# Kernel tuning notes

Measured on AMD Instinct MI355X. Metric: run time of the kernel, lower is better.

## Reference

```python
import jax, jax.numpy as jnp
import numpy as np

B, S, E, H = 4, 1024, 1024, 16
HD = E // H  # head_dim = 64


def setup_inputs() -> dict:
    key = jax.random.key(0)
    ks = jax.random.split(key, 7)
    return {
        "query": jax.random.normal(ks[0], (B, S, E), dtype=jnp.float32),
        "key": jax.random.normal(ks[1], (B, S, E), dtype=jnp.float32),
        "value": jax.random.normal(ks[2], (B, S, E), dtype=jnp.float32),
        # per-head Linear weights stacked: [H, head_dim, emb_dim] (torch Linear is y = x @ W^T)
        "Wq": jax.random.normal(ks[3], (H, HD, E), dtype=jnp.float32) * (E ** -0.5),
        "Wk": jax.random.normal(ks[4], (H, HD, E), dtype=jnp.float32) * (E ** -0.5),
        "Wv": jax.random.normal(ks[5], (H, HD, E), dtype=jnp.float32) * (E ** -0.5),
        "Wo": jax.random.normal(ks[6], (E, E), dtype=jnp.float32) * (E ** -0.5),
    }


def reference(query, key, value, Wq, Wk, Wv, Wo):
    # Project per head (all heads vectorized): [B,S,E] x [H,HD,E] -> [B,H,S,HD]
    Q = jnp.einsum('bse,hde->bhsd', query, Wq)
    K = jnp.einsum('bse,hde->bhsd', key, Wk)
    V = jnp.einsum('bse,hde->bhsd', value, Wv)
    scale = 1.0 / np.sqrt(HD)  # source divides by sqrt(emb_dim / n_head)
    scores = jnp.einsum('bhsd,bhtd->bhst', Q, K) * scale  # [B,H,S,S]
    p = jax.nn.softmax(scores, axis=-1)
    ctx = jnp.einsum('bhst,bhtd->bhsd', p, V)  # [B,H,S,HD]
    # concat heads along feature dim -> [B,S,E]
    concat = ctx.transpose(0, 2, 1, 3).reshape(query.shape[0], query.shape[1], -1)
    return concat @ Wo.T
```

## Files before the change

### kernel.cpp

```cpp
#include <hip/hip_runtime.h>

typedef __bf16 bf16_t;
typedef __bf16 bf16x4 __attribute__((ext_vector_type(4)));
typedef __bf16 bf16x8 __attribute__((ext_vector_type(8)));
typedef float f32x4 __attribute__((ext_vector_type(4)));
typedef short short4v __attribute__((ext_vector_type(4)));

#define E_DIM 1024
#define S_LEN 1024
#define NHEAD 16
#define HD_DIM 64
#define BATCH 4
#define TOKENS 4096

__device__ __forceinline__ void async_copy16(const bf16_t* g, bf16_t* l) {
    __builtin_amdgcn_global_load_lds((const __attribute__((address_space(1))) void*)g,
                                     (__attribute__((address_space(3))) void*)l,
                                     16, 0, 0);
}

__device__ __forceinline__ f32x4 pv_mfma(bf16x4 a, bf16x4 b, f32x4 c) {
#if __has_builtin(__builtin_amdgcn_mfma_f32_16x16x16_bf16)
    return __builtin_amdgcn_mfma_f32_16x16x16_bf16(a, b, c, 0, 0, 0);
#elif __has_builtin(__builtin_amdgcn_mfma_f32_16x16x16bf16_1k)
    short4v as, bs;
    __builtin_memcpy(&as, &a, 8);
    __builtin_memcpy(&bs, &b, 8);
    return __builtin_amdgcn_mfma_f32_16x16x16bf16_1k(as, bs, c, 0, 0, 0);
#else
    f32x4 d;
    asm volatile("v_mfma_f32_16x16x16_bf16 %0, %1, %2, %3\n\ts_nop 7\n\ts_nop 7"
                 : "=v"(d)
                 : "v"(a), "v"(b), "v"(c));
    return d;
#endif
}

__device__ __forceinline__ void stage_tiles(const bf16_t* gA, const bf16_t* gB,
                                            bf16_t* sAbuf, bf16_t* sBbuf,
                                            int wave, int k0) {
    const int K = 1024;
#pragma unroll
    for (int cc = 0; cc < 4; cc++) {
        int c = wave * 4 + cc;
        if (c < 8)
            async_copy16(gA + (size_t)c * 16 * K + k0, sAbuf + c * 16 * 32);
        else
            async_copy16(gB + (size_t)(c - 8) * 16 * K + k0, sBbuf + (c - 8) * 16 * 32);
    }
}

__global__ __launch_bounds__(256) void cast_all(const float* __restrict__ q,
                                                const float* __restrict__ k,
                                                const float* __restrict__ v,
                                                const float* __restrict__ wq,
                                                const float* __restrict__ wk,
                                                const float* __restrict__ wv,
                                                const float* __restrict__ wo,
                                                bf16_t* __restrict__ dst) {
    const size_t NX = (size_t)TOKENS * E_DIM;
    const size_t NW = (size_t)E_DIM * E_DIM;
    size_t i = ((size_t)blockIdx.x * 256 + threadIdx.x) * 8;
    const float* src;
    size_t off;
    if (i < 3 * NX) {
        int a = (int)(i >> 22);
        src = a == 0 ? q : (a == 1 ? k : v);
        off = i & (NX - 1);
    } else {
        size_t j = i - 3 * NX;
        int a = (int)(j >> 20);
        src = a == 0 ? wq : (a == 1 ? wk : (a == 2 ? wv : wo));
        off = j & (NW - 1);
    }
    float4 x = *(const float4*)(src + off);
    float4 y = *(const float4*)(src + off + 4);
    bf16x8 o;
    o[0] = (bf16_t)x.x; o[1] = (bf16_t)x.y; o[2] = (bf16_t)x.z; o[3] = (bf16_t)x.w;
    o[4] = (bf16_t)y.x; o[5] = (bf16_t)y.y; o[6] = (bf16_t)y.z; o[7] = (bf16_t)y.w;
    *(bf16x8*)(dst + i) = o;
}

__global__ __launch_bounds__(256, 3) void proj_gemm(const bf16_t* __restrict__ Xq,
                                                    const bf16_t* __restrict__ Xk,
                                                    const bf16_t* __restrict__ Xv,
                                                    const bf16_t* __restrict__ Wq,
                                                    const bf16_t* __restrict__ Wk,
                                                    const bf16_t* __restrict__ Wv,
                                                    bf16_t* __restrict__ Qp,
                                                    bf16_t* __restrict__ Kp,
                                                    bf16_t* __restrict__ Vp) {
    __shared__ bf16_t sA[3][128 * 32];
    __shared__ bf16_t sB[3][128 * 32];
    const int z = blockIdx.z;
    const bf16_t* A = z == 0 ? Xq : (z == 1 ? Xk : Xv);
    const bf16_t* B = z == 0 ? Wq : (z == 1 ? Wk : Wv);
    bf16_t* C = z == 0 ? Qp : (z == 1 ? Kp : Vp);
    const int N = 1024, K = 1024;
    const int lid = blockIdx.x + 8 * blockIdx.y;
    const int m0 = (((lid & 7) << 2) + ((lid >> 3) & 3)) * 128;
    const int n0 = (lid >> 5) * 128;

    const int tid = threadIdx.x;
    const int wave = tid >> 6, lane = tid & 63;
    const int quad = lane >> 4, l16 = lane & 15;
    const int wm = (wave >> 1) * 64, wn = (wave & 1) * 64;
    const int srow = lane >> 2, scol = (lane & 3) * 8;

    const bf16_t* gA = A + (size_t)(m0 + srow) * K + scol;
    const bf16_t* gB = B + (size_t)(n0 + srow) * K + scol;

    f32x4 acc[4][4];
    const f32x4 vzero = {0.f, 0.f, 0.f, 0.f};
#pragma unroll
    for (int mt = 0; mt < 4; mt++)
#pragma unroll
        for (int nt = 0; nt < 4; nt++) acc[mt][nt] = vzero;

#define PROJ_COMPUTE(cur)                                                             \
    {                                                                                 \
        bf16x8 af[4], bfr[4];                                                         \
        _Pragma("unroll") for (int mt = 0; mt < 4; mt++)                              \
            af[mt] = *(const bf16x8*)&sA[cur][(wm + mt * 16 + l16) * 32 + quad * 8];  \
        _Pragma("unroll") for (int nt = 0; nt < 4; nt++)                              \
            bfr[nt] = *(const bf16x8*)&sB[cur][(wn + nt * 16 + l16) * 32 + quad * 8]; \
        _Pragma("unroll") for (int mt = 0; mt < 4; mt++)                              \
            _Pragma("unroll") for (int nt = 0; nt < 4; nt++)                          \
                acc[mt][nt] = __builtin_amdgcn_mfma_f32_16x16x32_bf16(                \
                    af[mt], bfr[nt], acc[mt][nt], 0, 0, 0);                           \
    }

    stage_tiles(gA, gB, sA[0], sB[0], wave, 0);
    stage_tiles(gA, gB, sA[1], sB[1], wave, 32);
    stage_tiles(gA, gB, sA[2], sB[2], wave, 64);

    int cur = 0;
#pragma unroll 1
    for (int it = 0; it < 29; ++it) {
        asm volatile("s_waitcnt vmcnt(8)" ::: "memory");
        asm volatile("s_barrier" ::: "memory");
        PROJ_COMPUTE(cur);
        asm volatile("s_waitcnt lgkmcnt(0)" ::: "memory");
        asm volatile("s_barrier" ::: "memory");
        stage_tiles(gA, gB, sA[cur], sB[cur], wave, (it + 3) * 32);
        cur = cur == 2 ? 0 : cur + 1;
    }
    asm volatile("s_waitcnt vmcnt(8)" ::: "memory");
    asm volatile("s_barrier" ::: "memory");
    PROJ_COMPUTE(cur);
    cur = cur == 2 ? 0 : cur + 1;
    asm volatile("s_waitcnt vmcnt(4)" ::: "memory");
    asm volatile("s_barrier" ::: "memory");
    PROJ_COMPUTE(cur);
    cur = cur == 2 ? 0 : cur + 1;
    asm volatile("s_waitcnt vmcnt(0)" ::: "memory");
    asm volatile("s_barrier" ::: "memory");
    PROJ_COMPUTE(cur);
#undef PROJ_COMPUTE

#pragma unroll
    for (int mt = 0; mt < 4; mt++)
#pragma unroll
        for (int nt = 0; nt < 4; nt++)
#pragma unroll
            for (int r = 0; r < 4; r++) {
                int row = m0 + wm + mt * 16 + quad * 4 + r;
                int col = n0 + wn + nt * 16 + l16;
                C[(size_t)row * N + col] = (bf16_t)acc[mt][nt][r];
            }
}

__global__ __launch_bounds__(256, 3) void out_gemm(const bf16_t* __restrict__ A,
                                                   const bf16_t* __restrict__ B,
                                                   float* __restrict__ C) {
    __shared__ bf16_t sA[3][128 * 32];
    __shared__ bf16_t sB[3][128 * 32];
    const int N = 1024, K = 1024;
    const int lid = blockIdx.x + 8 * blockIdx.y;
    const int m0 = (((lid & 7) << 2) + ((lid >> 3) & 3)) * 128;
    const int n0 = (lid >> 5) * 128;

    const int tid = threadIdx.x;
    const int wave = tid >> 6, lane = tid & 63;
    const int quad = lane >> 4, l16 = lane & 15;
    const int wm = (wave >> 1) * 64, wn = (wave & 1) * 64;
    const int srow = lane >> 2, scol = (lane & 3) * 8;

    const bf16_t* gA = A + (size_t)(m0 + srow) * K + scol;
    const bf16_t* gB = B + (size_t)(n0 + srow) * K + scol;

    f32x4 acc[4][4];
    const f32x4 vzero = {0.f, 0.f, 0.f, 0.f};
#pragma unroll
    for (int mt = 0; mt < 4; mt++)
#pragma unroll
        for (int nt = 0; nt < 4; nt++) acc[mt][nt] = vzero;

#define OUT_COMPUTE(cur)                                                              \
    {                                                                                 \
        bf16x8 af[4], bfr[4];                                                         \
        _Pragma("unroll") for (int mt = 0; mt < 4; mt++)                              \
            af[mt] = *(const bf16x8*)&sA[cur][(wm + mt * 16 + l16) * 32 + quad * 8];  \
        _Pragma("unroll") for (int nt = 0; nt < 4; nt++)                              \
            bfr[nt] = *(const bf16x8*)&sB[cur][(wn + nt * 16 + l16) * 32 + quad * 8]; \
        _Pragma("unroll") for (int mt = 0; mt < 4; mt++)                              \
            _Pragma("unroll") for (int nt = 0; nt < 4; nt++)                          \
                acc[mt][nt] = __builtin_amdgcn_mfma_f32_16x16x32_bf16(                \
                    af[mt], bfr[nt], acc[mt][nt], 0, 0, 0);                           \
    }

    stage_tiles(gA, gB, sA[0], sB[0], wave, 0);
    stage_tiles(gA, gB, sA[1], sB[1], wave, 32);
    stage_tiles(gA, gB, sA[2], sB[2], wave, 64);

    int cur = 0;
#pragma unroll 1
    for (int it = 0; it < 29; ++it) {
        asm volatile("s_waitcnt vmcnt(8)" ::: "memory");
        asm volatile("s_barrier" ::: "memory");
        OUT_COMPUTE(cur);
        asm volatile("s_waitcnt lgkmcnt(0)" ::: "memory");
        asm volatile("s_barrier" ::: "memory");
        stage_tiles(gA, gB, sA[cur], sB[cur], wave, (it + 3) * 32);
        cur = cur == 2 ? 0 : cur + 1;
    }
    asm volatile("s_waitcnt vmcnt(8)" ::: "memory");
    asm volatile("s_barrier" ::: "memory");
    OUT_COMPUTE(cur);
    cur = cur == 2 ? 0 : cur + 1;
    asm volatile("s_waitcnt vmcnt(4)" ::: "memory");
    asm volatile("s_barrier" ::: "memory");
    OUT_COMPUTE(cur);
    cur = cur == 2 ? 0 : cur + 1;
    asm volatile("s_waitcnt vmcnt(0)" ::: "memory");
    asm volatile("s_barrier" ::: "memory");
    OUT_COMPUTE(cur);
#undef OUT_COMPUTE

#pragma unroll
    for (int mt = 0; mt < 4; mt++)
#pragma unroll
        for (int nt = 0; nt < 4; nt++)
#pragma unroll
            for (int r = 0; r < 4; r++) {
                int row = m0 + wm + mt * 16 + quad * 4 + r;
                int col = n0 + wn + nt * 16 + l16;
                C[(size_t)row * N + col] = acc[mt][nt][r];
            }
}

#define KP 72

__global__ __launch_bounds__(256, 2) void flash_attn(const bf16_t* __restrict__ Q,
                                                     const bf16_t* __restrict__ K,
                                                     const bf16_t* __restrict__ V,
                                                     bf16_t* __restrict__ O) {
    __shared__ bf16_t smem[2 * 64 * KP];
    bf16_t* sK = smem;
    bf16_t* sVt = smem + 64 * KP;

    const int tid = threadIdx.x;
    const int wave = tid >> 6, lane = tid & 63;
    const int quad = lane >> 4, l16 = lane & 15;
    const int qt = blockIdx.y >> 1;
    const int h = blockIdx.x * 2 + (blockIdx.y & 1);
    const int b = blockIdx.z;
    const size_t base = (size_t)b * S_LEN * E_DIM + h * HD_DIM;
    const float c_exp = 0.125f * 1.44269504089f;

    bf16x8 qf[2][2];
#pragma unroll
    for (int mt = 0; mt < 2; mt++) {
        const bf16_t* qp =
            Q + base + (size_t)(qt * 128 + wave * 32 + mt * 16 + l16) * E_DIM + quad * 8;
        qf[mt][0] = *(const bf16x8*)qp;
        qf[mt][1] = *(const bf16x8*)(qp + 32);
    }

    float lsum[2] = {0.f, 0.f};
    f32x4 acc[2][4];
    const f32x4 vzero = {0.f, 0.f, 0.f, 0.f};
#pragma unroll
    for (int mt = 0; mt < 2; mt++)
#pragma unroll
        for (int dt = 0; dt < 4; dt++) acc[mt][dt] = vzero;

    const int stg = tid & 7;

    for (int j0 = 0; j0 < S_LEN; j0 += 64) {
        __syncthreads();
#pragma unroll
        for (int it = 0; it < 2; it++) {
            int r = (tid >> 3) + it * 32;
            int c = stg * 8;
            bf16x8 kv = *(const bf16x8*)(K + base + (size_t)(j0 + r) * E_DIM + c);
            *(bf16x8*)&sK[r * KP + c] = kv;
            bf16x8 vv = *(const bf16x8*)(V + base + (size_t)(j0 + r) * E_DIM + c);
            int jb = (((r >> 2) ^ stg) << 2) | (r & 3);
#pragma unroll
            for (int i = 0; i < 8; i++) sVt[(c + i) * KP + jb] = vv[i];
        }
        __syncthreads();

        bf16x8 kf[4][2];
#pragma unroll
        for (int jt = 0; jt < 4; jt++) {
            kf[jt][0] = *(const bf16x8*)&sK[(jt * 16 + l16) * KP + quad * 8];
            kf[jt][1] = *(const bf16x8*)&sK[(jt * 16 + l16) * KP + 32 + quad * 8];
        }

        bf16x4 pb[2][4];
#pragma unroll
        for (int mt = 0; mt < 2; mt++)
#pragma unroll
            for (int jt = 0; jt < 4; jt++) {
                f32x4 s = vzero;
                s = __builtin_amdgcn_mfma_f32_16x16x32_bf16(kf[jt][0], qf[mt][0], s, 0, 0, 0);
                s = __builtin_amdgcn_mfma_f32_16x16x32_bf16(kf[jt][1], qf[mt][1], s, 0, 0, 0);
#pragma unroll
                for (int r = 0; r < 4; r++) {
                    float p = __builtin_amdgcn_exp2f(s[r] * c_exp);
                    lsum[mt] += p;
                    pb[mt][jt][r] = (bf16_t)p;
                }
            }

#pragma unroll
        for (int jt = 0; jt < 4; jt++)
#pragma unroll
            for (int dt = 0; dt < 4; dt++) {
                int cidx = (jt * 4 + quad) ^ (dt * 2 + (l16 >> 3));
                bf16x4 vf = *(const bf16x4*)&sVt[(dt * 16 + l16) * KP + cidx * 4];
#pragma unroll
                for (int mt = 0; mt < 2; mt++)
                    acc[mt][dt] = pv_mfma(vf, pb[mt][jt], acc[mt][dt]);
            }
    }

    float inv[2];
#pragma unroll
    for (int mt = 0; mt < 2; mt++) {
        lsum[mt] += __shfl_xor(lsum[mt], 16);
        lsum[mt] += __shfl_xor(lsum[mt], 32);
        inv[mt] = __builtin_amdgcn_rcpf(lsum[mt]);
    }

    __syncthreads();
    bf16_t* ep = smem + wave * 32 * KP;
#pragma unroll
    for (int mt = 0; mt < 2; mt++)
#pragma unroll
        for (int dt = 0; dt < 4; dt++)
#pragma unroll
            for (int r = 0; r < 4; r++)
                ep[(mt * 16 + l16) * KP + dt * 16 + quad * 4 + r] =
                    (bf16_t)(acc[mt][dt][r] * inv[mt]);
#pragma unroll
    for (int mt = 0; mt < 2; mt++)
#pragma unroll
        for (int c = 0; c < 2; c++) {
            int row = lane >> 2;
            int col = (lane & 3) * 8 + c * 32;
            bf16x8 oval = *(const bf16x8*)&ep[(mt * 16 + row) * KP + col];
            *(bf16x8*)&O[base + (size_t)(qt * 128 + wave * 32 + mt * 16 + row) * E_DIM + col] =
                oval;
        }
}

extern "C" void kernel_launch(void* const* d_in, const int* in_sizes, int n_in,
                              void* d_out, int out_size, void* d_ws, size_t ws_size,
                              hipStream_t stream) {
    const float* q  = (const float*)d_in[0];
    const float* k  = (const float*)d_in[1];
    const float* v  = (const float*)d_in[2];
    const float* wq = (const float*)d_in[3];
    const float* wk = (const float*)d_in[4];
    const float* wv = (const float*)d_in[5];
    const float* wo = (const float*)d_in[6];
    float* out = (float*)d_out;

    const int NX = TOKENS * E_DIM;
    const int NW = E_DIM * E_DIM;

    bf16_t* ws  = (bf16_t*)d_ws;
    bf16_t* Xq  = ws;
    bf16_t* Xk  = ws + (size_t)NX;
    bf16_t* Xv  = ws + (size_t)2 * NX;
    bf16_t* Wqb = ws + (size_t)3 * NX;
    bf16_t* Wkb = Wqb + NW;
    bf16_t* Wvb = Wkb + NW;
    bf16_t* Wob = Wvb + NW;
    bf16_t* Qp  = Wob + NW;
    bf16_t* Kp  = Qp + (size_t)NX;
    bf16_t* Vp  = Kp + (size_t)NX;
    bf16_t* ctx = Xq;

    cast_all<<<8192, 256, 0, stream>>>(q, k, v, wq, wk, wv, wo, Xq);

    proj_gemm<<<dim3(8, 32, 3), 256, 0, stream>>>(Xq, Xk, Xv, Wqb, Wkb, Wvb, Qp, Kp, Vp);

    flash_attn<<<dim3(8, 16, 4), 256, 0, stream>>>(Qp, Kp, Vp, ctx);

    out_gemm<<<dim3(8, 32), 256, 0, stream>>>(ctx, Wob, out);
}
```

Baseline: 185.9 us.

## Fuse activation fp32-to-bf16 cast into projection GEMM tile loads

The projection GEMM now loads fp32 activation tiles straight into LDS with async copies, using an XOR swizzle, and converts them to bf16 while building MFMA fragments. The cast kernel now only converts the weights. This removes a full read and write of the three activation tensors by a separate kernel. The cost is fp32 tiles that double the LDS footprint for A, which forces the pipeline from three stages down to two, plus conversion ALU work in the inner loop.

Measured after the change: 195.6 us. 1.05x slower.

```diff
diff --git a/kernel.cpp b/kernel.cpp
--- a/kernel.cpp
+++ b/kernel.cpp
@@ -13,7 +13,7 @@
 #define BATCH 4
 #define TOKENS 4096
 
-__device__ __forceinline__ void async_copy16(const bf16_t* g, bf16_t* l) {
+__device__ __forceinline__ void async_copy16(const void* g, void* l) {
     __builtin_amdgcn_global_load_lds((const __attribute__((address_space(1))) void*)g,
                                      (__attribute__((address_space(3))) void*)l,
                                      16, 0, 0);
@@ -50,29 +50,16 @@
     }
 }
 
-__global__ __launch_bounds__(256) void cast_all(const float* __restrict__ q,
-                                                const float* __restrict__ k,
-                                                const float* __restrict__ v,
-                                                const float* __restrict__ wq,
-                                                const float* __restrict__ wk,
-                                                const float* __restrict__ wv,
-                                                const float* __restrict__ wo,
-                                                bf16_t* __restrict__ dst) {
-    const size_t NX = (size_t)TOKENS * E_DIM;
+__global__ __launch_bounds__(256) void cast_w(const float* __restrict__ wq,
+                                              const float* __restrict__ wk,
+                                              const float* __restrict__ wv,
+                                              const float* __restrict__ wo,
+                                              bf16_t* __restrict__ dst) {
     const size_t NW = (size_t)E_DIM * E_DIM;
     size_t i = ((size_t)blockIdx.x * 256 + threadIdx.x) * 8;
-    const float* src;
-    size_t off;
-    if (i < 3 * NX) {
-        int a = (int)(i >> 22);
-        src = a == 0 ? q : (a == 1 ? k : v);
-        off = i & (NX - 1);
-    } else {
-        size_t j = i - 3 * NX;
-        int a = (int)(j >> 20);
-        src = a == 0 ? wq : (a == 1 ? wk : (a == 2 ? wv : wo));
-        off = j & (NW - 1);
-    }
+    int a = (int)(i >> 20);
+    const float* src = a == 0 ? wq : (a == 1 ? wk : (a == 2 ? wv : wo));
+    size_t off = i & (NW - 1);
     float4 x = *(const float4*)(src + off);
     float4 y = *(const float4*)(src + off + 4);
     bf16x8 o;
@@ -81,19 +68,19 @@
     *(bf16x8*)(dst + i) = o;
 }
 
-__global__ __launch_bounds__(256, 3) void proj_gemm(const bf16_t* __restrict__ Xq,
-                                                    const bf16_t* __restrict__ Xk,
-                                                    const bf16_t* __restrict__ Xv,
+__global__ __launch_bounds__(256, 3) void proj_gemm(const float* __restrict__ Xq,
+                                                    const float* __restrict__ Xk,
+                                                    const float* __restrict__ Xv,
                                                     const bf16_t* __restrict__ Wq,
                                                     const bf16_t* __restrict__ Wk,
                                                     const bf16_t* __restrict__ Wv,
                                                     bf16_t* __restrict__ Qp,
                                                     bf16_t* __restrict__ Kp,
                                                     bf16_t* __restrict__ Vp) {
-    __shared__ bf16_t sA[3][128 * 32];
-    __shared__ bf16_t sB[3][128 * 32];
+    __shared__ float sAf[2][128 * 32];
+    __shared__ bf16_t sB[2][128 * 32];
     const int z = blockIdx.z;
-    const bf16_t* A = z == 0 ? Xq : (z == 1 ? Xk : Xv);
+    const float* A = z == 0 ? Xq : (z == 1 ? Xk : Xv);
     const bf16_t* B = z == 0 ? Wq : (z == 1 ? Wk : Wv);
     bf16_t* C = z == 0 ? Qp : (z == 1 ? Kp : Vp);
     const int N = 1024, K = 1024;
@@ -105,10 +92,10 @@
     const int wave = tid >> 6, lane = tid & 63;
     const int quad = lane >> 4, l16 = lane & 15;
     const int wm = (wave >> 1) * 64, wn = (wave & 1) * 64;
-    const int srow = lane >> 2, scol = (lane & 3) * 8;
-
-    const bf16_t* gA = A + (size_t)(m0 + srow) * K + scol;
-    const bf16_t* gB = B + (size_t)(n0 + srow) * K + scol;
+
+    const int arow = lane >> 3;
+    const int acol = ((lane & 7) ^ ((arow & 3) << 1)) * 4;
+    const int brow = lane >> 2, bcol = (lane & 3) * 8;
 
     f32x4 acc[4][4];
     const f32x4 vzero = {0.f, 0.f, 0.f, 0.f};
@@ -117,45 +104,63 @@
 #pragma unroll
         for (int nt = 0; nt < 4; nt++) acc[mt][nt] = vzero;
 
-#define PROJ_COMPUTE(cur)                                                             \
-    {                                                                                 \
-        bf16x8 af[4], bfr[4];                                                         \
-        _Pragma("unroll") for (int mt = 0; mt < 4; mt++)                              \
-            af[mt] = *(const bf16x8*)&sA[cur][(wm + mt * 16 + l16) * 32 + quad * 8];  \
-        _Pragma("unroll") for (int nt = 0; nt < 4; nt++)                              \
-            bfr[nt] = *(const bf16x8*)&sB[cur][(wn + nt * 16 + l16) * 32 + quad * 8]; \
-        _Pragma("unroll") for (int mt = 0; mt < 4; mt++)                              \
-            _Pragma("unroll") for (int nt = 0; nt < 4; nt++)                          \
-                acc[mt][nt] = __builtin_amdgcn_mfma_f32_16x16x32_bf16(                \
-                    af[mt], bfr[nt], acc[mt][nt], 0, 0, 0);                           \
-    }
-
-    stage_tiles(gA, gB, sA[0], sB[0], wave, 0);
-    stage_tiles(gA, gB, sA[1], sB[1], wave, 32);
-    stage_tiles(gA, gB, sA[2], sB[2], wave, 64);
+#define PROJ_STAGE(buf, k0)                                                          \
+    {                                                                                \
+        _Pragma("unroll") for (int cc = 0; cc < 6; cc++) {                           \
+            int c = wave * 6 + cc;                                                   \
+            if (c < 16)                                                              \
+                async_copy16(A + (size_t)(m0 + c * 8 + arow) * K + (k0) + acol,      \
+                             &sAf[buf][c * 256]);                                    \
+            else {                                                                   \
+                int cb = c - 16;                                                     \
+                async_copy16(B + (size_t)(n0 + cb * 16 + brow) * K + (k0) + bcol,    \
+                             &sB[buf][cb * 512]);                                    \
+            }                                                                        \
+        }                                                                            \
+    }
+
+#define PROJ_COMPUTE(cur)                                                            \
+    {                                                                                \
+        bf16x8 af[4], bfr[4];                                                        \
+        _Pragma("unroll") for (int mt = 0; mt < 4; mt++) {                           \
+            int r = wm + mt * 16 + l16;                                              \
+            const float* pa = &sAf[cur][r * 32 + ((quad ^ (l16 & 3)) * 8)];          \
+            f32x4 a0 = *(const f32x4*)pa;                                            \
+            f32x4 a1 = *(const f32x4*)(pa + 4);                                      \
+            bf16x8 t;                                                                \
+            _Pragma("unroll") for (int i = 0; i < 4; i++) {                          \
+                t[i] = (bf16_t)a0[i];                                                \
+                t[4 + i] = (bf16_t)a1[i];                                            \
+            }                                                                        \
+            af[mt] = t;                                                              \
+        }                                                                            \
+        _Pragma("unroll") for (int nt = 0; nt < 4; nt++)                             \
+            bfr[nt] = *(const bf16x8*)&sB[cur][(wn + nt * 16 + l16) * 32 + quad * 8];\
+        _Pragma("unroll") for (int mt = 0; mt < 4; mt++)                             \
+            _Pragma("unroll") for (int nt = 0; nt < 4; nt++)                         \
+                acc[mt][nt] = __builtin_amdgcn_mfma_f32_16x16x32_bf16(               \
+                    af[mt], bfr[nt], acc[mt][nt], 0, 0, 0);                          \
+    }
+
+    PROJ_STAGE(0, 0);
+    PROJ_STAGE(1, 32);
 
     int cur = 0;
 #pragma unroll 1
-    for (int it = 0; it < 29; ++it) {
-        asm volatile("s_waitcnt vmcnt(8)" ::: "memory");
+    for (int it = 0; it < 31; ++it) {
+        asm volatile("s_waitcnt vmcnt(6)" ::: "memory");
         asm volatile("s_barrier" ::: "memory");
         PROJ_COMPUTE(cur);
         asm volatile("s_waitcnt lgkmcnt(0)" ::: "memory");
         asm volatile("s_barrier" ::: "memory");
-        stage_tiles(gA, gB, sA[cur], sB[cur], wave, (it + 3) * 32);
-        cur = cur == 2 ? 0 : cur + 1;
-    }
-    asm volatile("s_waitcnt vmcnt(8)" ::: "memory");
-    asm volatile("s_barrier" ::: "memory");
-    PROJ_COMPUTE(cur);
-    cur = cur == 2 ? 0 : cur + 1;
-    asm volatile("s_waitcnt vmcnt(4)" ::: "memory");
-    asm volatile("s_barrier" ::: "memory");
-    PROJ_COMPUTE(cur);
-    cur = cur == 2 ? 0 : cur + 1;
+        int knext = (it + 2) * 32;
+        if (knext < K) PROJ_STAGE(cur, knext);
+        cur ^= 1;
+    }
     asm volatile("s_waitcnt vmcnt(0)" ::: "memory");
     asm volatile("s_barrier" ::: "memory");
     PROJ_COMPUTE(cur);
+#undef PROJ_STAGE
 #undef PROJ_COMPUTE
 
 #pragma unroll
@@ -383,21 +388,18 @@
     const int NW = E_DIM * E_DIM;
 
     bf16_t* ws  = (bf16_t*)d_ws;
-    bf16_t* Xq  = ws;
-    bf16_t* Xk  = ws + (size_t)NX;
-    bf16_t* Xv  = ws + (size_t)2 * NX;
-    bf16_t* Wqb = ws + (size_t)3 * NX;
+    bf16_t* Wqb = ws;
     bf16_t* Wkb = Wqb + NW;
     bf16_t* Wvb = Wkb + NW;
     bf16_t* Wob = Wvb + NW;
     bf16_t* Qp  = Wob + NW;
     bf16_t* Kp  = Qp + (size_t)NX;
     bf16_t* Vp  = Kp + (size_t)NX;
-    bf16_t* ctx = Xq;
-
-    cast_all<<<8192, 256, 0, stream>>>(q, k, v, wq, wk, wv, wo, Xq);
-
-    proj_gemm<<<dim3(8, 32, 3), 256, 0, stream>>>(Xq, Xk, Xv, Wqb, Wkb, Wvb, Qp, Kp, Vp);
+    bf16_t* ctx = Vp + (size_t)NX;
+
+    cast_w<<<2048, 256, 0, stream>>>(wq, wk, wv, wo, Wqb);
+
+    proj_gemm<<<dim3(8, 32, 3), 256, 0, stream>>>(q, k, v, Wqb, Wkb, Wvb, Qp, Kp, Vp);
 
     flash_attn<<<dim3(8, 16, 4), 256, 0, stream>>>(Qp, Kp, Vp, ctx);
 
```
